# Kernel tuning notes

Hardware: AMD Instinct MI355X
Metric: run time of the kernel (lower is better)

## Reference

```python
import jax, jax.numpy as jnp
import numpy as np

B, C, H, W = 8, 256, 64, 64
CELLS_PER_IMAGE = 16
N = B * CELLS_PER_IMAGE  # total cells


def setup_inputs() -> dict:
    key = jax.random.key(0)
    k1, k2 = jax.random.split(key)
    feature_maps = jax.random.normal(k1, (B, C, H, W), dtype=jnp.float32)
    # dense-ish boolean cell masks; with 4096 pixels per mask every cell is nonempty
    cell_masks = jax.random.bernoulli(k2, p=0.25, shape=(N, H, W))
    cell_counts = jnp.full((B,), CELLS_PER_IMAGE, dtype=jnp.int32)
    return {"feature_maps": feature_maps, "cell_masks": cell_masks, "cell_counts": cell_counts}


def reference(feature_maps, cell_masks, cell_counts):
    # method='max', positions=False (constructor defaults).
    # Map each cell to its source image: repeat(arange(B), counts) with a
    # static total length so it is jit-compatible.
    n_cells = cell_masks.shape[0]
    batch = feature_maps.shape[0]
    cell_batch = jnp.repeat(jnp.arange(batch), cell_counts, total_repeat_length=n_cells)
    x = feature_maps[cell_batch]  # (N, C, H, W) gathered per cell
    neg_inf = jnp.asarray(-jnp.inf, x.dtype)
    masked = jnp.where(cell_masks[:, None, :, :], x, neg_inf)
    # max over the masked pixels of each cell -> (N, C)
    return jnp.max(masked, axis=(2, 3))
```

## Files before the change

kernel.cpp:

```cpp
#include <hip/hip_runtime.h>
#include <hip/hip_bf16.h>


#define HW    4096
#define BIMG  8
#define CCH   256
#define NCELL 128

__device__ __forceinline__ void cell_range(const int* counts, int b, int& start, int& cnt) {
    start = 0;
    for (int i = 0; i < b; ++i) start += counts[i];
    if (start > NCELL) start = NCELL;
    cnt = counts[b];
    if (b == BIMG - 1 && start + cnt < NCELL) cnt = NCELL - start;
    if (cnt > 16) cnt = 16;
    if (start + cnt > NCELL) cnt = NCELL - start;
    if (cnt < 0) cnt = 0;
}

__global__ __launch_bounds__(256)
void pack_masks(const void* __restrict__ maskv,
                const int* __restrict__ counts,
                unsigned short* __restrict__ packed) {
    const int idx = blockIdx.x * blockDim.x + threadIdx.x;
    const int tid = threadIdx.x;
    const int b = idx >> 12;
    const int p = idx & (HW - 1);

    __shared__ int s_msize;
    if (tid < 64) {
        const unsigned* mw = (const unsigned*)maskv;
        unsigned ow = mw[tid * 4] | mw[tid * 4 + 1] | mw[tid * 4 + 2] | mw[tid * 4 + 3];
        #pragma unroll
        for (int d = 32; d >= 1; d >>= 1) ow |= __shfl_down(ow, d, 64);
        if (tid == 0) {
            unsigned or0 = ow & 0xFFu, or1 = (ow >> 8) & 0xFFu;
            int s;
            if (or1 == 0)                         s = 4;
            else if (or0 == 0x80 || or0 == 0x00)  s = 2;
            else                                  s = 1;
            s_msize = s;
        }
    }
    __syncthreads();
    const int msize = s_msize;

    int start, cnt;
    cell_range(counts, b, start, cnt);

    unsigned w = 0;
    if (msize == 2) {
        const unsigned short* mh = (const unsigned short*)maskv;
        for (int j = 0; j < cnt; ++j)
            w |= (mh[(size_t)(start + j) * HW + p] ? 1u : 0u) << j;
    } else if (msize == 4) {
        const unsigned* mw = (const unsigned*)maskv;
        for (int j = 0; j < cnt; ++j)
            w |= (mw[(size_t)(start + j) * HW + p] ? 1u : 0u) << j;
    } else {
        const unsigned char* mb = (const unsigned char*)maskv;
        for (int j = 0; j < cnt; ++j)
            w |= (mb[(size_t)(start + j) * HW + p] ? 1u : 0u) << j;
    }
    packed[idx] = (unsigned short)w;
}

__global__ __launch_bounds__(256, 4)
void roipool_main(const void* __restrict__ featv,
                  const unsigned short* __restrict__ packed,
                  const int* __restrict__ counts,
                  void* __restrict__ outv) {
    const int c   = blockIdx.x;
    const int b   = blockIdx.y;
    const int tid = threadIdx.x;
    const float NEG = -__builtin_inff();
    const unsigned NEGI = 0xFF800000u;

    __shared__ int s_fbf16;
    if (tid < 64) {
        const unsigned* fw_ = (const unsigned*)featv;
        unsigned w = fw_[tid];
        unsigned eb = (w >> 8) & 0x7F;
        unsigned long long bm = __ballot(eb >= 0x3B && eb <= 0x41);
        if (tid == 0) s_fbf16 = (__popcll(bm) >= 48);
    }
    __syncthreads();
    const int fbf16 = s_fbf16;

    int start, cnt;
    cell_range(counts, b, start, cnt);

    const int p0 = tid * 16;

    uint4 pa = *(const uint4*)(packed + ((size_t)b << 12) + p0);
    uint4 pb = *(const uint4*)(packed + ((size_t)b << 12) + p0 + 8);
    unsigned pmw[8] = {pa.x, pa.y, pa.z, pa.w, pb.x, pb.y, pb.z, pb.w};

    unsigned pe[8], po[8];
    if (fbf16) {
        const unsigned short* fp = (const unsigned short*)featv
                                 + (((size_t)(b * CCH + c)) << 12) + p0;
        uint4 f0 = *(const uint4*)(fp);
        uint4 f1 = *(const uint4*)(fp + 8);
        unsigned w8[8] = {f0.x, f0.y, f0.z, f0.w, f1.x, f1.y, f1.z, f1.w};
        #pragma unroll
        for (int k = 0; k < 8; ++k) {
            pe[k] = w8[k] << 16;
            po[k] = w8[k] & 0xFFFF0000u;
        }
    } else {
        const float* fp = (const float*)featv + (((size_t)(b * CCH + c)) << 12) + p0;
        #pragma unroll
        for (int q = 0; q < 4; ++q) {
            uint4 a = *(const uint4*)(fp + q * 4);
            pe[q * 2]     = a.x; po[q * 2]     = a.y;
            pe[q * 2 + 1] = a.z; po[q * 2 + 1] = a.w;
        }
    }

    float vmax[16];
    #pragma unroll
    for (int j = 0; j < 16; ++j) vmax[j] = NEG;

    #pragma unroll
    for (int k = 0; k < 8; ++k) {
        const unsigned fe = pe[k], fo = po[k];
        const unsigned mw = pmw[k];
        #pragma unroll
        for (int j = 0; j < 16; ++j) {
            unsigned m0 = (unsigned)(((int)(mw << (31 - j))) >> 31);
            unsigned m1 = (unsigned)(((int)(mw << (15 - j))) >> 31);
            float s0 = __uint_as_float((fe & m0) | (NEGI & ~m0));
            float s1 = __uint_as_float((fo & m1) | (NEGI & ~m1));
            vmax[j] = fmaxf(fmaxf(vmax[j], s0), s1);
        }
    }

    __shared__ float red[256 * 17];
    __shared__ float red2[16 * 17];
    #pragma unroll
    for (int j = 0; j < 16; ++j) red[tid * 17 + j] = vmax[j];
    __syncthreads();
    {
        const int jj = tid & 15;
        const int g  = tid >> 4;
        float m = NEG;
        #pragma unroll
        for (int r = 0; r < 16; ++r)
            m = fmaxf(m, red[(g * 16 + r) * 17 + jj]);
        red2[g * 17 + jj] = m;
    }
    __syncthreads();
    if (tid < 16) {
        float m2 = NEG;
        #pragma unroll
        for (int g2 = 0; g2 < 16; ++g2)
            m2 = fmaxf(m2, red2[g2 * 17 + tid]);
        if (tid < cnt) {
            size_t oi = (size_t)(start + tid) * CCH + c;
            if (fbf16) ((__hip_bfloat16*)outv)[oi] = __float2bfloat16(m2);
            else       ((float*)outv)[oi] = m2;
        }
    }
}

extern "C" void kernel_launch(void* const* d_in, const int* in_sizes, int n_in,
                              void* d_out, int out_size, void* d_ws, size_t ws_size,
                              hipStream_t stream) {
    const void* feat  = d_in[0];
    const void* masks = d_in[1];
    const int* counts = (const int*)d_in[2];
    unsigned short* packed = (unsigned short*)d_ws;

    pack_masks<<<(BIMG * HW) / 256, 256, 0, stream>>>(masks, counts, packed);

    dim3 grid(CCH, BIMG);
    roipool_main<<<grid, 256, 0, stream>>>(feat, packed, counts, d_out);
}
```

Baseline: 86.45 us.

## Map one wavefront per channel and reduce with shuffles instead of LDS

The main kernel now gives each 64-lane wavefront a whole (image, channel) pair and processes 64 pixels per lane. Partial maxima are combined with cross-lane xor shuffles rather than a shared-memory tree with two block barriers. The mask-packing kernel runs 64-thread blocks, detects the mask dtype per wave with no LDS or sync, and fully unrolls the common 16-cell case. The per-lane work and register pressure grow (launch bounds lowered to 2 blocks per CU), and the 16 parallel shuffle chains add cross-lane traffic.

```diff
diff --git a/kernel.cpp b/kernel.cpp
--- a/kernel.cpp
+++ b/kernel.cpp
@@ -18,149 +18,160 @@
     if (cnt < 0) cnt = 0;
 }
 
-__global__ __launch_bounds__(256)
+__global__ __launch_bounds__(64)
 void pack_masks(const void* __restrict__ maskv,
                 const int* __restrict__ counts,
                 unsigned short* __restrict__ packed) {
-    const int idx = blockIdx.x * blockDim.x + threadIdx.x;
     const int tid = threadIdx.x;
+    const int idx = blockIdx.x * 64 + tid;
     const int b = idx >> 12;
     const int p = idx & (HW - 1);
 
-    __shared__ int s_msize;
-    if (tid < 64) {
-        const unsigned* mw = (const unsigned*)maskv;
-        unsigned ow = mw[tid * 4] | mw[tid * 4 + 1] | mw[tid * 4 + 2] | mw[tid * 4 + 3];
-        #pragma unroll
-        for (int d = 32; d >= 1; d >>= 1) ow |= __shfl_down(ow, d, 64);
-        if (tid == 0) {
-            unsigned or0 = ow & 0xFFu, or1 = (ow >> 8) & 0xFFu;
-            int s;
-            if (or1 == 0)                         s = 4;
-            else if (or0 == 0x80 || or0 == 0x00)  s = 2;
-            else                                  s = 1;
-            s_msize = s;
-        }
-    }
-    __syncthreads();
-    const int msize = s_msize;
+    const unsigned* mw0 = (const unsigned*)maskv;
+    unsigned ow = mw0[tid * 4] | mw0[tid * 4 + 1] | mw0[tid * 4 + 2] | mw0[tid * 4 + 3];
+    #pragma unroll
+    for (int d = 1; d < 64; d <<= 1) ow |= __shfl_xor(ow, d, 64);
+    const unsigned or0 = ow & 0xFFu, or1 = (ow >> 8) & 0xFFu;
+    int msize;
+    if (or1 == 0)                        msize = 4;
+    else if (or0 == 0x80 || or0 == 0x00) msize = 2;
+    else                                 msize = 1;
 
     int start, cnt;
     cell_range(counts, b, start, cnt);
 
     unsigned w = 0;
     if (msize == 2) {
-        const unsigned short* mh = (const unsigned short*)maskv;
-        for (int j = 0; j < cnt; ++j)
-            w |= (mh[(size_t)(start + j) * HW + p] ? 1u : 0u) << j;
+        const unsigned short* mh = (const unsigned short*)maskv + (size_t)start * HW + p;
+        if (cnt == 16) {
+            #pragma unroll
+            for (int j = 0; j < 16; ++j)
+                w |= (mh[(size_t)j * HW] ? 1u : 0u) << j;
+        } else {
+            for (int j = 0; j < cnt; ++j)
+                w |= (mh[(size_t)j * HW] ? 1u : 0u) << j;
+        }
     } else if (msize == 4) {
-        const unsigned* mw = (const unsigned*)maskv;
-        for (int j = 0; j < cnt; ++j)
-            w |= (mw[(size_t)(start + j) * HW + p] ? 1u : 0u) << j;
+        const unsigned* mw = (const unsigned*)maskv + (size_t)start * HW + p;
+        if (cnt == 16) {
+            #pragma unroll
+            for (int j = 0; j < 16; ++j)
+                w |= (mw[(size_t)j * HW] ? 1u : 0u) << j;
+        } else {
+            for (int j = 0; j < cnt; ++j)
+                w |= (mw[(size_t)j * HW] ? 1u : 0u) << j;
+        }
     } else {
-        const unsigned char* mb = (const unsigned char*)maskv;
-        for (int j = 0; j < cnt; ++j)
-            w |= (mb[(size_t)(start + j) * HW + p] ? 1u : 0u) << j;
+        const unsigned char* mb = (const unsigned char*)maskv + (size_t)start * HW + p;
+        if (cnt == 16) {
+            #pragma unroll
+            for (int j = 0; j < 16; ++j)
+                w |= (mb[(size_t)j * HW] ? 1u : 0u) << j;
+        } else {
+            for (int j = 0; j < cnt; ++j)
+                w |= (mb[(size_t)j * HW] ? 1u : 0u) << j;
+        }
     }
     packed[idx] = (unsigned short)w;
 }
 
-__global__ __launch_bounds__(256, 4)
+__global__ __launch_bounds__(256, 2)
 void roipool_main(const void* __restrict__ featv,
                   const unsigned short* __restrict__ packed,
                   const int* __restrict__ counts,
                   void* __restrict__ outv) {
-    const int c   = blockIdx.x;
-    const int b   = blockIdx.y;
     const int tid = threadIdx.x;
+    const int l   = tid & 63;
+    const int bc  = blockIdx.x * 4 + (tid >> 6);
+    const int c   = bc & (CCH - 1);
+    const int b   = bc >> 8;
     const float NEG = -__builtin_inff();
     const unsigned NEGI = 0xFF800000u;
 
-    __shared__ int s_fbf16;
-    if (tid < 64) {
-        const unsigned* fw_ = (const unsigned*)featv;
-        unsigned w = fw_[tid];
-        unsigned eb = (w >> 8) & 0x7F;
-        unsigned long long bm = __ballot(eb >= 0x3B && eb <= 0x41);
-        if (tid == 0) s_fbf16 = (__popcll(bm) >= 48);
-    }
-    __syncthreads();
-    const int fbf16 = s_fbf16;
+    const unsigned* fw_ = (const unsigned*)featv;
+    const unsigned w0 = fw_[l];
+    const unsigned eb = (w0 >> 8) & 0x7F;
+    const unsigned long long bm = __ballot(eb >= 0x3B && eb <= 0x41);
+    const int fbf16 = (__popcll(bm) >= 48);
 
     int start, cnt;
     cell_range(counts, b, start, cnt);
 
-    const int p0 = tid * 16;
-
-    uint4 pa = *(const uint4*)(packed + ((size_t)b << 12) + p0);
-    uint4 pb = *(const uint4*)(packed + ((size_t)b << 12) + p0 + 8);
-    unsigned pmw[8] = {pa.x, pa.y, pa.z, pa.w, pb.x, pb.y, pb.z, pb.w};
-
-    unsigned pe[8], po[8];
-    if (fbf16) {
-        const unsigned short* fp = (const unsigned short*)featv
-                                 + (((size_t)(b * CCH + c)) << 12) + p0;
-        uint4 f0 = *(const uint4*)(fp);
-        uint4 f1 = *(const uint4*)(fp + 8);
-        unsigned w8[8] = {f0.x, f0.y, f0.z, f0.w, f1.x, f1.y, f1.z, f1.w};
-        #pragma unroll
-        for (int k = 0; k < 8; ++k) {
-            pe[k] = w8[k] << 16;
-            po[k] = w8[k] & 0xFFFF0000u;
-        }
-    } else {
-        const float* fp = (const float*)featv + (((size_t)(b * CCH + c)) << 12) + p0;
-        #pragma unroll
-        for (int q = 0; q < 4; ++q) {
-            uint4 a = *(const uint4*)(fp + q * 4);
-            pe[q * 2]     = a.x; po[q * 2]     = a.y;
-            pe[q * 2 + 1] = a.z; po[q * 2 + 1] = a.w;
-        }
-    }
+    const unsigned short* pk = packed + ((size_t)b << 12);
+    uint4 pm[8];
+    #pragma unroll
+    for (int i = 0; i < 8; ++i)
+        pm[i] = *(const uint4*)(pk + (i * 64 + l) * 8);
 
     float vmax[16];
     #pragma unroll
     for (int j = 0; j < 16; ++j) vmax[j] = NEG;
 
-    #pragma unroll
-    for (int k = 0; k < 8; ++k) {
-        const unsigned fe = pe[k], fo = po[k];
-        const unsigned mw = pmw[k];
+    if (fbf16) {
+        const unsigned short* fp = (const unsigned short*)featv
+                                 + (((size_t)(b * CCH + c)) << 12);
         #pragma unroll
-        for (int j = 0; j < 16; ++j) {
-            unsigned m0 = (unsigned)(((int)(mw << (31 - j))) >> 31);
-            unsigned m1 = (unsigned)(((int)(mw << (15 - j))) >> 31);
-            float s0 = __uint_as_float((fe & m0) | (NEGI & ~m0));
-            float s1 = __uint_as_float((fo & m1) | (NEGI & ~m1));
-            vmax[j] = fmaxf(fmaxf(vmax[j], s0), s1);
+        for (int i = 0; i < 8; ++i) {
+            uint4 f = *(const uint4*)(fp + (i * 64 + l) * 8);
+            const unsigned fw4[4] = {f.x, f.y, f.z, f.w};
+            const unsigned mw4[4] = {pm[i].x, pm[i].y, pm[i].z, pm[i].w};
+            #pragma unroll
+            for (int k = 0; k < 4; ++k) {
+                const unsigned fe = fw4[k] << 16;
+                const unsigned fo = fw4[k] & 0xFFFF0000u;
+                const unsigned mw = mw4[k];
+                #pragma unroll
+                for (int j = 0; j < 16; ++j) {
+                    unsigned m0 = (unsigned)(((int)(mw << (31 - j))) >> 31);
+                    unsigned m1 = (unsigned)(((int)(mw << (15 - j))) >> 31);
+                    float s0 = __uint_as_float((fe & m0) | (NEGI & ~m0));
+                    float s1 = __uint_as_float((fo & m1) | (NEGI & ~m1));
+                    vmax[j] = fmaxf(fmaxf(vmax[j], s0), s1);
+                }
+            }
+        }
+    } else {
+        const float* fp = (const float*)featv + (((size_t)(b * CCH + c)) << 12);
+        #pragma unroll
+        for (int i = 0; i < 8; ++i) {
+            const float* cp = fp + (i * 64 + l) * 8;
+            uint4 q0 = *(const uint4*)(cp);
+            uint4 q1 = *(const uint4*)(cp + 4);
+            const unsigned pe4[4] = {q0.x, q0.z, q1.x, q1.z};
+            const unsigned po4[4] = {q0.y, q0.w, q1.y, q1.w};
+            const unsigned mw4[4] = {pm[i].x, pm[i].y, pm[i].z, pm[i].w};
+            #pragma unroll
+            for (int k = 0; k < 4; ++k) {
+                const unsigned fe = pe4[k];
+                const unsigned fo = po4[k];
+                const unsigned mw = mw4[k];
+                #pragma unroll
+                for (int j = 0; j < 16; ++j) {
+                    unsigned m0 = (unsigned)(((int)(mw << (31 - j))) >> 31);
+                    unsigned m1 = (unsigned)(((int)(mw << (15 - j))) >> 31);
+                    float s0 = __uint_as_float((fe & m0) | (NEGI & ~m0));
+                    float s1 = __uint_as_float((fo & m1) | (NEGI & ~m1));
+                    vmax[j] = fmaxf(fmaxf(vmax[j], s0), s1);
+                }
+            }
         }
     }
 
-    __shared__ float red[256 * 17];
-    __shared__ float red2[16 * 17];
     #pragma unroll
-    for (int j = 0; j < 16; ++j) red[tid * 17 + j] = vmax[j];
-    __syncthreads();
-    {
-        const int jj = tid & 15;
-        const int g  = tid >> 4;
-        float m = NEG;
+    for (int d = 1; d < 64; d <<= 1) {
         #pragma unroll
-        for (int r = 0; r < 16; ++r)
-            m = fmaxf(m, red[(g * 16 + r) * 17 + jj]);
-        red2[g * 17 + jj] = m;
+        for (int j = 0; j < 16; ++j)
+            vmax[j] = fmaxf(vmax[j], __shfl_xor(vmax[j], d, 64));
     }
-    __syncthreads();
-    if (tid < 16) {
-        float m2 = NEG;
-        #pragma unroll
-        for (int g2 = 0; g2 < 16; ++g2)
-            m2 = fmaxf(m2, red2[g2 * 17 + tid]);
-        if (tid < cnt) {
-            size_t oi = (size_t)(start + tid) * CCH + c;
-            if (fbf16) ((__hip_bfloat16*)outv)[oi] = __float2bfloat16(m2);
-            else       ((float*)outv)[oi] = m2;
-        }
+
+    float v = vmax[0];
+    #pragma unroll
+    for (int j = 1; j < 16; ++j) v = (l == j) ? vmax[j] : v;
+
+    if (l < 16 && l < cnt) {
+        const size_t oi = (size_t)(start + l) * CCH + c;
+        if (fbf16) ((__hip_bfloat16*)outv)[oi] = __float2bfloat16(v);
+        else       ((float*)outv)[oi]          = v;
     }
 }
 
@@ -172,8 +183,7 @@
     const int* counts = (const int*)d_in[2];
     unsigned short* packed = (unsigned short*)d_ws;
 
-    pack_masks<<<(BIMG * HW) / 256, 256, 0, stream>>>(masks, counts, packed);
+    pack_masks<<<(BIMG * HW) / 64, 64, 0, stream>>>(masks, counts, packed);
 
-    dim3 grid(CCH, BIMG);
-    roipool_main<<<grid, 256, 0, stream>>>(feat, packed, counts, d_out);
+    roipool_main<<<(BIMG * CCH) / 4, 256, 0, stream>>>(feat, packed, counts, d_out);
 }
```

New measurement: 117.9 us. 1.36x slower.
